# Kernel tuning notes

Hardware: AMD Instinct MI355X
Metric: run time of the kernel (lower is better)

## Reference

```python
import jax, jax.numpy as jnp
import numpy as np

EMBED = 1024
HEAD = 128
B, T = 4, 4096


def setup_inputs() -> dict:
    key = jax.random.key(0)
    k1, k2, k3, k4 = jax.random.split(key, 4)
    context = jax.random.normal(k1, (B, T, EMBED), dtype=jnp.float32)
    # nn.Linear(embedding_size, head_size, bias=False): y = x @ W^T; store W^T as [C, H]
    s = 1.0 / np.sqrt(EMBED)
    Wk = jax.random.normal(k2, (EMBED, HEAD), dtype=jnp.float32) * s
    Wq = jax.random.normal(k3, (EMBED, HEAD), dtype=jnp.float32) * s
    Wv = jax.random.normal(k4, (EMBED, HEAD), dtype=jnp.float32) * s
    return {"context": context, "Wk": Wk, "Wq": Wq, "Wv": Wv}


def reference(context, Wk, Wq, Wv):
    Bc, Tc, C = context.shape
    k = jnp.einsum("btc,ch->bth", context, Wk)
    q = jnp.einsum("btc,ch->bth", context, Wq)
    v = jnp.einsum("btc,ch->bth", context, Wv)
    # NOTE: original scales by 1/sqrt(C) (embedding size), not 1/sqrt(head_size)
    scale = 1.0 / jnp.sqrt(jnp.float32(C))
    scores = jnp.einsum("bqh,bkh->bqk", q, k) * scale  # [B, T, T]
    causal = jnp.tril(jnp.ones((Tc, Tc), dtype=bool))
    scores = jnp.where(causal, scores, -jnp.inf)
    attn = jax.nn.softmax(scores, axis=-1)
    # dropout_rate = 0.0 (eval-mode): no-op
    out = jnp.einsum("bqk,bkh->bqh", attn, v)
    return out
```

## Files before the change

### kernel.cpp

```cpp
#include <hip/hip_runtime.h>
#include <cstdint>
#include <cstddef>

#define EMBED 1024
#define HEAD  128
#define BATCH 4
#define SEQ   4096
#define KSC   0.04508422f

typedef __attribute__((ext_vector_type(4))) float f32x4;
typedef __attribute__((ext_vector_type(16))) float f32x16;
typedef __attribute__((ext_vector_type(8))) short s16x8;
typedef __attribute__((ext_vector_type(4))) int i32x4;
typedef __attribute__((ext_vector_type(4))) unsigned short u16x4;

__device__ __forceinline__ unsigned short f2bf(float f) {
    union { float f; unsigned u; } v; v.f = f;
    unsigned r = v.u + 0x7fffu + ((v.u >> 16) & 1u);
    return (unsigned short)(r >> 16);
}

__device__ __forceinline__ int cvtpk(float lo, float hi_) {
    int r;
    asm("v_cvt_pk_bf16_f32 %0, %1, %2" : "=v"(r) : "v"(lo), "v"(hi_));
    return r;
}

__device__ __forceinline__ void gload16(const void* g, void* l) {
    __builtin_amdgcn_global_load_lds(
        (const __attribute__((address_space(1))) unsigned int*)g,
        (__attribute__((address_space(3))) unsigned int*)l, 16, 0, 0);
}

__global__ __launch_bounds__(256) void wt_kernel(const float* __restrict__ Wq,
                                                 const float* __restrict__ Wk,
                                                 const float* __restrict__ Wv,
                                                 unsigned short* __restrict__ Wt) {
    __shared__ __align__(16) float Lw[64 * 132];
    const int tid = threadIdx.x;
    const int sel = blockIdx.x >> 4;
    const int kb  = blockIdx.x & 15;
    const int k0  = kb * 64;
    const float* W = (sel == 0) ? Wq : (sel == 1) ? Wk : Wv;
    #pragma unroll
    for (int it = 0; it < 8; ++it) {
        int c = tid + it * 256;
        int kk = c >> 5, hc = c & 31;
        *(f32x4*)&Lw[kk * 132 + hc * 4] =
            *(const f32x4*)(W + (size_t)(k0 + kk) * HEAD + hc * 4);
    }
    __syncthreads();
    #pragma unroll
    for (int it = 0; it < 4; ++it) {
        int c = tid + it * 256;
        int h = c >> 3, sl = c & 7;
        int phys = sl ^ (h & 7);
        int p0 = cvtpk(Lw[(sl * 8 + 0) * 132 + h], Lw[(sl * 8 + 1) * 132 + h]);
        int p1 = cvtpk(Lw[(sl * 8 + 2) * 132 + h], Lw[(sl * 8 + 3) * 132 + h]);
        int p2 = cvtpk(Lw[(sl * 8 + 4) * 132 + h], Lw[(sl * 8 + 5) * 132 + h]);
        int p3 = cvtpk(Lw[(sl * 8 + 6) * 132 + h], Lw[(sl * 8 + 7) * 132 + h]);
        i32x4 pk = {p0, p1, p2, p3};
        *(s16x8*)(Wt + (size_t)sel * 131072 + kb * 8192 + h * 64 + phys * 8) = *(s16x8*)&pk;
    }
}

__global__ __launch_bounds__(256) void proj_kernel(const float* __restrict__ ctx,
                                                   const unsigned short* __restrict__ Wt,
                                                   unsigned short* __restrict__ Qb,
                                                   unsigned short* __restrict__ Kb,
                                                   unsigned short* __restrict__ Vtb) {
    __shared__ __align__(16) short As[64 * 72];
    __shared__ __align__(16) short Bs[128 * 64];
    const int tid = threadIdx.x;
    const int lane = tid & 63, w = tid >> 6;
    const int wr = w >> 1, wc = w & 1;
    const int lr = lane & 15, lk = lane >> 4;
    const int m0 = blockIdx.x * 64;
    const int sel = blockIdx.y;
    const unsigned short* Wts = Wt + (size_t)sel * 131072;

    f32x4 zero = {0.f, 0.f, 0.f, 0.f};
    f32x4 acc[2][4];
    #pragma unroll
    for (int i = 0; i < 2; ++i)
        #pragma unroll
        for (int jn = 0; jn < 4; ++jn) acc[i][jn] = zero;

    for (int kkb = 0; kkb < 16; ++kkb) {
        __syncthreads();
        const char* gb = (const char*)Wts + kkb * 16384;
        #pragma unroll
        for (int i = 0; i < 4; ++i) {
            int chunk = w * 4 + i;
            gload16(gb + chunk * 1024 + lane * 16, (char*)Bs + chunk * 1024);
        }
        const int kk = kkb * 64;
        #pragma unroll
        for (int t = 0; t < 2; ++t) {
            int c = tid + t * 256;
            int row = c >> 3, cg = c & 7;
            const float* src = ctx + (size_t)(m0 + row) * EMBED + kk + cg * 8;
            f32x4 x0 = *(const f32x4*)src;
            f32x4 x1 = *(const f32x4*)(src + 4);
            int p0 = cvtpk(x0[0], x0[1]);
            int p1 = cvtpk(x0[2], x0[3]);
            int p2 = cvtpk(x1[0], x1[1]);
            int p3 = cvtpk(x1[2], x1[3]);
            i32x4 pk = {p0, p1, p2, p3};
            *(s16x8*)&As[row * 72 + cg * 8] = *(s16x8*)&pk;
        }
        __syncthreads();
        s16x8 af[2][2], bfr[4][2];
        #pragma unroll
        for (int mi = 0; mi < 2; ++mi)
            #pragma unroll
            for (int k2 = 0; k2 < 2; ++k2)
                af[mi][k2] = *(const s16x8*)&As[(wr * 32 + mi * 16 + lr) * 72 + k2 * 32 + lk * 8];
        #pragma unroll
        for (int ni = 0; ni < 4; ++ni)
            #pragma unroll
            for (int k2 = 0; k2 < 2; ++k2) {
                int rB = wc * 64 + ni * 16 + lr;
                int phys = (k2 * 4 + lk) ^ (rB & 7);
                bfr[ni][k2] = *(const s16x8*)((const char*)Bs + rB * 128 + phys * 16);
            }
        #pragma unroll
        for (int k2 = 0; k2 < 2; ++k2)
            #pragma unroll
            for (int mi = 0; mi < 2; ++mi)
                #pragma unroll
                for (int ni = 0; ni < 4; ++ni)
                    acc[mi][ni] = __builtin_amdgcn_mfma_f32_16x16x32_bf16(af[mi][k2], bfr[ni][k2], acc[mi][ni], 0, 0, 0);
    }

    if (sel == 2) {
        #pragma unroll
        for (int mi = 0; mi < 2; ++mi) {
            int t0r = m0 + wr * 32 + mi * 16 + lk * 4;
            int b = t0r >> 12, tl = t0r & (SEQ - 1);
            #pragma unroll
            for (int ni = 0; ni < 4; ++ni) {
                int col = wc * 64 + ni * 16 + lr;
                u16x4 vv;
                #pragma unroll
                for (int r = 0; r < 4; ++r) vv[r] = f2bf(acc[mi][ni][r]);
                *(u16x4*)(Vtb + ((size_t)(b * HEAD + col)) * SEQ + tl) = vv;
            }
        }
    } else {
        unsigned short* outp = sel ? Kb : Qb;
        const float sc = sel ? 1.0f : KSC;
        #pragma unroll
        for (int mi = 0; mi < 2; ++mi) {
            int row = m0 + wr * 32 + mi * 16 + lk * 4;
            #pragma unroll
            for (int ni = 0; ni < 4; ++ni) {
                int col = wc * 64 + ni * 16 + lr;
                #pragma unroll
                for (int r = 0; r < 4; ++r)
                    outp[(size_t)(row + r) * HEAD + col] = f2bf(acc[mi][ni][r] * sc);
            }
        }
    }
}

__global__ __launch_bounds__(256, 2) void attn_kernel(const unsigned short* __restrict__ Q,
                                                      const unsigned short* __restrict__ K,
                                                      const unsigned short* __restrict__ Vt,
                                                      unsigned short* __restrict__ po,
                                                      float* __restrict__ pml) {
    __shared__ __align__(16) char smem[32768];
    const int tid = threadIdx.x;
    const int lane = tid & 63, w = tid >> 6;
    const int l31 = lane & 31, hi = lane >> 5;
    const int hi16 = hi << 4;

    const int b = blockIdx.x / 272;
    int t = blockIdx.x % 272;
    int qt = 0, cum = 0;
    while (cum + ((qt >> 1) + 1) <= t) { cum += (qt >> 1) + 1; ++qt; }
    const int c = t - cum;
    const int nj = min(4, 2 * qt + 2 - 4 * c);
    const int kb0 = c * 256;
    const int slot = b * 272 + cum + c;

    const unsigned short* qp = Q + ((size_t)(b * SEQ + qt * 128 + w * 32 + l31)) * HEAD + hi * 8;
    s16x8 qf[8];
    #pragma unroll
    for (int dt = 0; dt < 8; ++dt) qf[dt] = *(const s16x8*)(qp + dt * 16);

    f32x16 o0, o1, o2, o3;
    #pragma unroll
    for (int r = 0; r < 16; ++r) { o0[r] = 0.f; o1[r] = 0.f; o2[r] = 0.f; o3[r] = 0.f; }
    float m_run = -1e30f, l_run = 0.f;

    const int krow = tid >> 4, kch = tid & 15;
    const int vdr  = tid >> 3, vch = tid & 7;

    s16x8 kst[4], vst[4];
    #pragma unroll
    for (int p = 0; p < 4; ++p) {
        kst[p] = *(const s16x8*)(K + ((size_t)(b * SEQ + kb0 + krow + p * 16)) * HEAD + kch * 8);
        vst[p] = *(const s16x8*)(Vt + ((size_t)(b * HEAD + vdr + p * 32)) * SEQ + kb0 + vch * 8);
    }
    #pragma unroll
    for (int p = 0; p < 4; ++p) {
        int r0 = krow + p * 16;
        *(s16x8*)(smem + r0 * 256 + ((kch * 16) ^ ((r0 & 7) << 4))) = kst[p];
        int d0 = vdr + p * 32;
        *(s16x8*)(smem + 16384 + d0 * 128 + ((vch * 16) ^ ((d0 & 7) << 4))) = vst[p];
    }
    __syncthreads();

    for (int j = 0; j < nj; ++j) {
        const int kb = kb0 + j * 64;
        if (j + 1 < nj) {
            int kbn = kb + 64;
            #pragma unroll
            for (int p = 0; p < 4; ++p) {
                kst[p] = *(const s16x8*)(K + ((size_t)(b * SEQ + kbn + krow + p * 16)) * HEAD + kch * 8);
                vst[p] = *(const s16x8*)(Vt + ((size_t)(b * HEAD + vdr + p * 32)) * SEQ + kbn + vch * 8);
            }
        }

        f32x16 st0, st1;
        #pragma unroll
        for (int r = 0; r < 16; ++r) { st0[r] = 0.f; st1[r] = 0.f; }
        const int sw = (l31 & 7) << 4;
        const char* kbase0 = smem + l31 * 256;
        const char* kbase1 = kbase0 + 32 * 256;
        __builtin_amdgcn_s_setprio(1);
        #pragma unroll
        for (int dt = 0; dt < 8; ++dt) {
            s16x8 ka0 = *(const s16x8*)(kbase0 + ((dt * 32 + hi16) ^ sw));
            s16x8 ka1 = *(const s16x8*)(kbase1 + ((dt * 32 + hi16) ^ sw));
            st0 = __builtin_amdgcn_mfma_f32_32x32x16_bf16(ka0, qf[dt], st0, 0, 0, 0);
            st1 = __builtin_amdgcn_mfma_f32_32x32x16_bf16(ka1, qf[dt], st1, 0, 0, 0);
        }
        __builtin_amdgcn_s_setprio(0);

        if (4 * c + j >= 2 * qt) {
            const int qg = qt * 128 + w * 32 + l31;
            #pragma unroll
            for (int r = 0; r < 16; ++r) {
                int crow = (r & 3) + 8 * (r >> 2) + 4 * hi;
                if (kb + crow > qg)      st0[r] = -3e37f;
                if (kb + 32 + crow > qg) st1[r] = -3e37f;
            }
        }

        float mx = st0[0];
        #pragma unroll
        for (int r = 1; r < 16; ++r) mx = fmaxf(mx, st0[r]);
        #pragma unroll
        for (int r = 0; r < 16; ++r) mx = fmaxf(mx, st1[r]);
        mx = fmaxf(mx, __shfl_xor(mx, 32));
        if (!__all(mx <= m_run + 8.0f)) {
            float mn = fmaxf(m_run, mx);
            float f = exp2f(m_run - mn);
            l_run *= f;
            int fi = __float_as_int(f);
            #pragma unroll
            for (int r = 0; r < 16; ++r) {
                int srcb = 4 * ((r & 3) + 8 * (r >> 2)) + 16 * hi;
                float fr = __int_as_float(__builtin_amdgcn_ds_bpermute(srcb, fi));
                o0[r] *= fr; o1[r] *= fr; o2[r] *= fr; o3[r] *= fr;
            }
            m_run = mn;
        }
        float rs = 0.f;
        #pragma unroll
        for (int r = 0; r < 16; ++r) {
            st0[r] = exp2f(st0[r] - m_run); rs += st0[r];
            st1[r] = exp2f(st1[r] - m_run); rs += st1[r];
        }
        rs += __shfl_xor(rs, 32);
        l_run += rs;

        int a0 = cvtpk(st0[0], st0[1]),   b0 = cvtpk(st0[4], st0[5]);
        int a1 = cvtpk(st0[2], st0[3]),   b1 = cvtpk(st0[6], st0[7]);
        int a2 = cvtpk(st0[8], st0[9]),   b2 = cvtpk(st0[12], st0[13]);
        int a3 = cvtpk(st0[10], st0[11]), b3 = cvtpk(st0[14], st0[15]);
        int a4 = cvtpk(st1[0], st1[1]),   b4 = cvtpk(st1[4], st1[5]);
        int a5 = cvtpk(st1[2], st1[3]),   b5 = cvtpk(st1[6], st1[7]);
        int a6 = cvtpk(st1[8], st1[9]),   b6 = cvtpk(st1[12], st1[13]);
        int a7 = cvtpk(st1[10], st1[11]), b7 = cvtpk(st1[14], st1[15]);
        asm volatile("v_permlane32_swap_b32 %0, %1" : "+v"(a0), "+v"(b0));
        asm volatile("v_permlane32_swap_b32 %0, %1" : "+v"(a1), "+v"(b1));
        asm volatile("v_permlane32_swap_b32 %0, %1" : "+v"(a2), "+v"(b2));
        asm volatile("v_permlane32_swap_b32 %0, %1" : "+v"(a3), "+v"(b3));
        asm volatile("v_permlane32_swap_b32 %0, %1" : "+v"(a4), "+v"(b4));
        asm volatile("v_permlane32_swap_b32 %0, %1" : "+v"(a5), "+v"(b5));
        asm volatile("v_permlane32_swap_b32 %0, %1" : "+v"(a6), "+v"(b6));
        asm volatile("v_permlane32_swap_b32 %0, %1" : "+v"(a7), "+v"(b7));
        i32x4 pw0 = {a0, a1, b0, b1}; s16x8 pa0 = *(s16x8*)&pw0;
        i32x4 pw1 = {a2, a3, b2, b3}; s16x8 pa1 = *(s16x8*)&pw1;
        i32x4 pw2 = {a4, a5, b4, b5}; s16x8 pa2 = *(s16x8*)&pw2;
        i32x4 pw3 = {a6, a7, b6, b7}; s16x8 pa3 = *(s16x8*)&pw3;

        __builtin_amdgcn_s_setprio(1);
        #define PV_NT(oo, nt) { \
            const int vr = (nt) * 32 + l31; \
            const int vsw = (vr & 7) << 4; \
            const char* vb = smem + 16384 + vr * 128; \
            oo = __builtin_amdgcn_mfma_f32_32x32x16_bf16(pa0, *(const s16x8*)(vb + ((0  + hi16) ^ vsw)), oo, 0, 0, 0); \
            oo = __builtin_amdgcn_mfma_f32_32x32x16_bf16(pa1, *(const s16x8*)(vb + ((32 + hi16) ^ vsw)), oo, 0, 0, 0); \
            oo = __builtin_amdgcn_mfma_f32_32x32x16_bf16(pa2, *(const s16x8*)(vb + ((64 + hi16) ^ vsw)), oo, 0, 0, 0); \
            oo = __builtin_amdgcn_mfma_f32_32x32x16_bf16(pa3, *(const s16x8*)(vb + ((96 + hi16) ^ vsw)), oo, 0, 0, 0); }
        PV_NT(o0, 0) PV_NT(o1, 1) PV_NT(o2, 2) PV_NT(o3, 3)
        #undef PV_NT
        __builtin_amdgcn_s_setprio(0);

        if (j + 1 < nj) {
            __syncthreads();
            #pragma unroll
            for (int p = 0; p < 4; ++p) {
                int r0 = krow + p * 16;
                *(s16x8*)(smem + r0 * 256 + ((kch * 16) ^ ((r0 & 7) << 4))) = kst[p];
                int d0 = vdr + p * 32;
                *(s16x8*)(smem + 16384 + d0 * 128 + ((vch * 16) ^ ((d0 & 7) << 4))) = vst[p];
            }
            __syncthreads();
        }
    }

    __syncthreads();
    short* os = (short*)smem;
    #define STORE_NT(oo, nt) { \
        _Pragma("unroll") \
        for (int r = 0; r < 16; ++r) { \
            int qin = w * 32 + (r & 3) + 8 * (r >> 2) + 4 * hi; \
            os[qin * 128 + (nt) * 32 + l31] = (short)f2bf(oo[r]); \
        } }
    STORE_NT(o0, 0) STORE_NT(o1, 1) STORE_NT(o2, 2) STORE_NT(o3, 3)
    #undef STORE_NT
    unsigned short* pob = po + (size_t)slot * 16384 + w * 4096;
    const short* osw = os + w * 4096;
    #pragma unroll
    for (int jj = 0; jj < 8; ++jj) {
        s16x8 v = *(const s16x8*)(osw + jj * 512 + lane * 8);
        *(s16x8*)(pob + jj * 512 + lane * 8) = v;
    }
    if (lane < 32) {
        float* pm = pml + (size_t)slot * 256 + (w * 32 + lane) * 2;
        pm[0] = m_run; pm[1] = l_run;
    }
}

__global__ __launch_bounds__(256) void combine_kernel(const unsigned short* __restrict__ po,
                                                      const float* __restrict__ pml,
                                                      float* __restrict__ out) {
    const int tid = threadIdx.x;
    const int row = blockIdx.x * 8 + (tid >> 5);
    const int l32 = tid & 31;
    const int b = row >> 12, q = row & 4095;
    const int qt = q >> 7, qr = q & 127;
    const int nc = (q >> 8) + 1;
    const int cum = ((qt >> 1) + (qt & 1)) * ((qt >> 1) + 1);
    const size_t bslot = (size_t)b * 272 + cum;

    float M = -1e30f;
    for (int cc = 0; cc < nc; ++cc)
        M = fmaxf(M, pml[(bslot + cc) * 256 + qr * 2]);
    float L = 0.f;
    f32x4 acc = {0.f, 0.f, 0.f, 0.f};
    for (int cc = 0; cc < nc; ++cc) {
        const float* pm = pml + (bslot + cc) * 256 + qr * 2;
        float wgt = exp2f(pm[0] - M);
        L += wgt * pm[1];
        u16x4 x = *(const u16x4*)(po + (bslot + cc) * 16384 + qr * 128 + l32 * 4);
        #pragma unroll
        for (int e = 0; e < 4; ++e) {
            union { unsigned u; float f; } cv; cv.u = ((unsigned)x[e]) << 16;
            acc[e] += wgt * cv.f;
        }
    }
    float inv = 1.f / L;
    f32x4 y = {acc[0] * inv, acc[1] * inv, acc[2] * inv, acc[3] * inv};
    *(f32x4*)(out + (size_t)row * HEAD + l32 * 4) = y;
}

extern "C" void kernel_launch(void* const* d_in, const int* in_sizes, int n_in,
                              void* d_out, int out_size, void* d_ws, size_t ws_size,
                              hipStream_t stream) {
    const float* ctx = (const float*)d_in[0];
    const float* Wk  = (const float*)d_in[1];
    const float* Wq  = (const float*)d_in[2];
    const float* Wv  = (const float*)d_in[3];
    float* out = (float*)d_out;

    unsigned short* Wt  = (unsigned short*)d_ws;
    unsigned short* Qb  = Wt + 3 * 131072;
    unsigned short* Kb  = Qb + 2097152;
    unsigned short* Vtb = Kb + 2097152;
    unsigned short* po  = Vtb + 2097152;
    float* pml = (float*)(po + (size_t)1088 * 16384);

    wt_kernel<<<48, 256, 0, stream>>>(Wq, Wk, Wv, Wt);
    proj_kernel<<<dim3(256, 3), 256, 0, stream>>>(ctx, Wt, Qb, Kb, Vtb);
    attn_kernel<<<1088, 256, 0, stream>>>(Qb, Kb, Vtb, po, pml);
    combine_kernel<<<2048, 256, 0, stream>>>(po, pml, out);
}
```

Baseline: 165.5 us.

## Fuse Q, K and V projections into one block sharing the context tile

New measurement: 171.8 us, median of 2. 3.8% more time.

```diff
diff --git a/kernel.cpp b/kernel.cpp
--- a/kernel.cpp
+++ b/kernel.cpp
@@ -64,42 +64,38 @@
     }
 }
 
-__global__ __launch_bounds__(256) void proj_kernel(const float* __restrict__ ctx,
+__global__ __launch_bounds__(512) void proj_kernel(const float* __restrict__ ctx,
                                                    const unsigned short* __restrict__ Wt,
                                                    unsigned short* __restrict__ Qb,
                                                    unsigned short* __restrict__ Kb,
                                                    unsigned short* __restrict__ Vtb) {
     __shared__ __align__(16) short As[64 * 72];
-    __shared__ __align__(16) short Bs[128 * 64];
+    __shared__ __align__(16) short Bs[3 * 128 * 64];
     const int tid = threadIdx.x;
     const int lane = tid & 63, w = tid >> 6;
-    const int wr = w >> 1, wc = w & 1;
+    const int wr = w >> 2, wc = w & 3;
     const int lr = lane & 15, lk = lane >> 4;
     const int m0 = blockIdx.x * 64;
-    const int sel = blockIdx.y;
-    const unsigned short* Wts = Wt + (size_t)sel * 131072;
 
     f32x4 zero = {0.f, 0.f, 0.f, 0.f};
-    f32x4 acc[2][4];
+    f32x4 acc[2][6];
     #pragma unroll
     for (int i = 0; i < 2; ++i)
         #pragma unroll
-        for (int jn = 0; jn < 4; ++jn) acc[i][jn] = zero;
-
-    for (int kkb = 0; kkb < 16; ++kkb) {
+        for (int jn = 0; jn < 6; ++jn) acc[i][jn] = zero;
+
+    for (int kb = 0; kb < 16; ++kb) {
         __syncthreads();
-        const char* gb = (const char*)Wts + kkb * 16384;
-        #pragma unroll
-        for (int i = 0; i < 4; ++i) {
-            int chunk = w * 4 + i;
-            gload16(gb + chunk * 1024 + lane * 16, (char*)Bs + chunk * 1024);
-        }
-        const int kk = kkb * 64;
-        #pragma unroll
-        for (int t = 0; t < 2; ++t) {
-            int c = tid + t * 256;
-            int row = c >> 3, cg = c & 7;
-            const float* src = ctx + (size_t)(m0 + row) * EMBED + kk + cg * 8;
+        #pragma unroll
+        for (int i = 0; i < 6; ++i) {
+            int c = w * 6 + i;
+            int sel = c >> 4, within = c & 15;
+            gload16((const char*)Wt + sel * 262144 + kb * 16384 + within * 1024 + lane * 16,
+                    (char*)Bs + c * 1024);
+        }
+        {
+            int row = tid >> 3, cg = tid & 7;
+            const float* src = ctx + (size_t)(m0 + row) * EMBED + kb * 64 + cg * 8;
             f32x4 x0 = *(const f32x4*)src;
             f32x4 x1 = *(const f32x4*)(src + 4);
             int p0 = cvtpk(x0[0], x0[1]);
@@ -110,55 +106,46 @@
             *(s16x8*)&As[row * 72 + cg * 8] = *(s16x8*)&pk;
         }
         __syncthreads();
-        s16x8 af[2][2], bfr[4][2];
-        #pragma unroll
-        for (int mi = 0; mi < 2; ++mi)
-            #pragma unroll
-            for (int k2 = 0; k2 < 2; ++k2)
-                af[mi][k2] = *(const s16x8*)&As[(wr * 32 + mi * 16 + lr) * 72 + k2 * 32 + lk * 8];
-        #pragma unroll
-        for (int ni = 0; ni < 4; ++ni)
-            #pragma unroll
-            for (int k2 = 0; k2 < 2; ++k2) {
-                int rB = wc * 64 + ni * 16 + lr;
+        #pragma unroll
+        for (int k2 = 0; k2 < 2; ++k2) {
+            s16x8 af[2], bfr[6];
+            #pragma unroll
+            for (int mi = 0; mi < 2; ++mi)
+                af[mi] = *(const s16x8*)&As[(wr * 32 + mi * 16 + lr) * 72 + k2 * 32 + lk * 8];
+            #pragma unroll
+            for (int ni = 0; ni < 6; ++ni) {
+                int col = wc * 96 + ni * 16 + lr;
+                int sel = col >> 7, rB = col & 127;
                 int phys = (k2 * 4 + lk) ^ (rB & 7);
-                bfr[ni][k2] = *(const s16x8*)((const char*)Bs + rB * 128 + phys * 16);
-            }
-        #pragma unroll
-        for (int k2 = 0; k2 < 2; ++k2)
+                bfr[ni] = *(const s16x8*)(Bs + sel * 8192 + rB * 64 + phys * 8);
+            }
             #pragma unroll
             for (int mi = 0; mi < 2; ++mi)
                 #pragma unroll
-                for (int ni = 0; ni < 4; ++ni)
-                    acc[mi][ni] = __builtin_amdgcn_mfma_f32_16x16x32_bf16(af[mi][k2], bfr[ni][k2], acc[mi][ni], 0, 0, 0);
-    }
-
-    if (sel == 2) {
-        #pragma unroll
-        for (int mi = 0; mi < 2; ++mi) {
-            int t0r = m0 + wr * 32 + mi * 16 + lk * 4;
-            int b = t0r >> 12, tl = t0r & (SEQ - 1);
-            #pragma unroll
-            for (int ni = 0; ni < 4; ++ni) {
-                int col = wc * 64 + ni * 16 + lr;
+                for (int ni = 0; ni < 6; ++ni)
+                    acc[mi][ni] = __builtin_amdgcn_mfma_f32_16x16x32_bf16(af[mi], bfr[ni], acc[mi][ni], 0, 0, 0);
+        }
+    }
+
+    #pragma unroll
+    for (int mi = 0; mi < 2; ++mi) {
+        int rowBase = m0 + wr * 32 + mi * 16 + lk * 4;
+        #pragma unroll
+        for (int ni = 0; ni < 6; ++ni) {
+            int col = wc * 96 + ni * 16 + lr;
+            int sel = col >> 7, cIn = col & 127;
+            if (sel == 2) {
+                int b = rowBase >> 12, tl = rowBase & (SEQ - 1);
                 u16x4 vv;
                 #pragma unroll
                 for (int r = 0; r < 4; ++r) vv[r] = f2bf(acc[mi][ni][r]);
-                *(u16x4*)(Vtb + ((size_t)(b * HEAD + col)) * SEQ + tl) = vv;
-            }
-        }
-    } else {
-        unsigned short* outp = sel ? Kb : Qb;
-        const float sc = sel ? 1.0f : KSC;
-        #pragma unroll
-        for (int mi = 0; mi < 2; ++mi) {
-            int row = m0 + wr * 32 + mi * 16 + lk * 4;
-            #pragma unroll
-            for (int ni = 0; ni < 4; ++ni) {
-                int col = wc * 64 + ni * 16 + lr;
+                *(u16x4*)(Vtb + ((size_t)(b * HEAD + cIn)) * SEQ + tl) = vv;
+            } else {
+                unsigned short* outp = sel ? Kb : Qb;
+                float sc = sel ? 1.0f : KSC;
                 #pragma unroll
                 for (int r = 0; r < 4; ++r)
-                    outp[(size_t)(row + r) * HEAD + col] = f2bf(acc[mi][ni][r] * sc);
+                    outp[(size_t)(rowBase + r) * HEAD + cIn] = f2bf(acc[mi][ni][r] * sc);
             }
         }
     }
@@ -397,7 +384,7 @@
     float* pml = (float*)(po + (size_t)1088 * 16384);
 
     wt_kernel<<<48, 256, 0, stream>>>(Wq, Wk, Wv, Wt);
-    proj_kernel<<<dim3(256, 3), 256, 0, stream>>>(ctx, Wt, Qb, Kb, Vtb);
+    proj_kernel<<<256, 512, 0, stream>>>(ctx, Wt, Qb, Kb, Vtb);
     attn_kernel<<<1088, 256, 0, stream>>>(Qb, Kb, Vtb, po, pml);
     combine_kernel<<<2048, 256, 0, stream>>>(po, pml, out);
 }
```
